# Kernel tuning notes

Hardware: AMD Instinct MI355X
Metric: run time of the kernel (lower is better)

The kernel has to match this reference:

```python
import jax, jax.numpy as jnp
import numpy as np

NUM_TEAMS = 100000
INPUT_SIZE = 128
HIDDEN = 128
NUM_MATCHES = 1000000
OUT = 3


def setup_inputs() -> dict:
    key = jax.random.key(0)
    ks = jax.random.split(key, 10)
    s_ih = 1.0 / np.sqrt(HIDDEN)
    inputs = jax.random.normal(ks[0], (NUM_TEAMS, INPUT_SIZE), dtype=jnp.float32)
    hx = jax.random.normal(ks[1], (NUM_TEAMS, HIDDEN), dtype=jnp.float32)
    cx = jax.random.normal(ks[2], (NUM_TEAMS, HIDDEN), dtype=jnp.float32)
    matches = jax.random.randint(ks[3], (NUM_MATCHES, 2), 0, NUM_TEAMS, dtype=jnp.int64)
    W_ih = jax.random.uniform(ks[4], (4 * HIDDEN, INPUT_SIZE), jnp.float32, -s_ih, s_ih)
    W_hh = jax.random.uniform(ks[5], (4 * HIDDEN, HIDDEN), jnp.float32, -s_ih, s_ih)
    b_ih = jax.random.uniform(ks[6], (4 * HIDDEN,), jnp.float32, -s_ih, s_ih)
    b_hh = jax.random.uniform(ks[7], (4 * HIDDEN,), jnp.float32, -s_ih, s_ih)
    s_o = 1.0 / np.sqrt(2 * HIDDEN)
    W_out = jax.random.uniform(ks[8], (OUT, 2 * HIDDEN), jnp.float32, -s_o, s_o)
    b_out = jax.random.uniform(ks[9], (OUT,), jnp.float32, -s_o, s_o)
    return {"inputs": inputs, "hx": hx, "cx": cx, "matches": matches,
            "W_ih": W_ih, "W_hh": W_hh, "b_ih": b_ih, "b_hh": b_hh,
            "W_out": W_out, "b_out": b_out}


def reference(inputs, hx, cx, matches, W_ih, W_hh, b_ih, b_hh, W_out, b_out):
    # Batched LSTMCell step across all teams (replaces per-team Python loop).
    gates = inputs @ W_ih.T + b_ih + hx @ W_hh.T + b_hh  # [T, 4H]
    i_g, f_g, g_g, o_g = jnp.split(gates, 4, axis=1)
    c_new = jax.nn.sigmoid(f_g) * cx + jax.nn.sigmoid(i_g) * jnp.tanh(g_g)
    h_new = jax.nn.sigmoid(o_g) * jnp.tanh(c_new)  # [T, H]
    # Fused gather + concat + linear + softmax for all matches.
    home = h_new[matches[:, 0]]  # [M, H]
    away = h_new[matches[:, 1]]  # [M, H]
    feat = jnp.concatenate([home, away], axis=1)  # [M, 2H]
    logits = feat @ W_out.T + b_out  # [M, 3]
    pmf = jax.nn.softmax(logits, axis=-1)
    return pmf
```

## Files before the change

kernel.cpp:

```cpp
#include <hip/hip_runtime.h>
#include <hip/hip_bf16.h>

typedef __bf16 bf16x8 __attribute__((ext_vector_type(8)));
typedef float f32x4 __attribute__((ext_vector_type(4)));

#define NUM_TEAMS 100000
#define NUM_MATCHES 1000000
#define LOG2E 1.4426950408889634f
#define NWG 1563
#define XQ 195
#define XR 3

__device__ __forceinline__ unsigned short f2bf(float x) {
    __hip_bfloat16 h = __float2bfloat16(x);
    return reinterpret_cast<unsigned short&>(h);
}
__device__ __forceinline__ unsigned int cvtpk(float a, float b) {
    unsigned int r;
    asm("v_cvt_pk_bf16_f32 %0, %1, %2" : "=v"(r) : "v"(a), "v"(b));
    return r;
}
__device__ __forceinline__ float exp2_(float x) {
    float r; asm("v_exp_f32 %0, %1" : "=v"(r) : "v"(x)); return r;
}
__device__ __forceinline__ float rcp_(float x) {
    float r; asm("v_rcp_f32 %0, %1" : "=v"(r) : "v"(x)); return r;
}
__device__ __forceinline__ void load_lds16(const float* g, float* l) {
    __builtin_amdgcn_global_load_lds(
        (const __attribute__((address_space(1))) void*)g,
        (__attribute__((address_space(3))) void*)l, 16, 0, 0);
}

__global__ __launch_bounds__(256) void prep_kernel(
    const float* __restrict__ W_ih, const float* __restrict__ W_hh,
    const float* __restrict__ b_ih, const float* __restrict__ b_hh,
    unsigned short* __restrict__ Wpk, float* __restrict__ biasc)
{
    int gid = blockIdx.x * 256 + threadIdx.x;
    int e = gid & 7;
    int chunk = gid >> 3;
    int l15 = chunk & 15;
    int l4 = (chunk >> 4) & 3;
    int rest = chunk >> 6;
    int ks = rest & 7;
    int gate = (rest >> 3) & 3;
    int G = rest >> 5;
    int row = gate * 128 + G * 16 + l15;
    int k = ks * 32 + l4 * 8 + e;
    float v = (k < 128) ? W_ih[row * 128 + k] : W_hh[row * 128 + (k - 128)];
    Wpk[gid] = f2bf(v);
    if (gid < 512) {
        float b = b_ih[gid] + b_hh[gid];
        float scale = ((gid >> 7) == 2) ? (2.0f * LOG2E) : (-LOG2E);
        biasc[gid] = b * scale;
    }
}

__global__ __launch_bounds__(512, 4) void lstm_kernel(
    const float* __restrict__ inputs, const float* __restrict__ hx,
    const float* __restrict__ cx, const unsigned short* __restrict__ Wpk,
    const float* __restrict__ biasc, const float* __restrict__ W_out,
    float* __restrict__ projP)
{
    __shared__ __align__(16) float Af[64 * 256];
    __shared__ float Wlds[768];
    const int tid = threadIdx.x;

    const int orig = blockIdx.x;
    const int xcd = orig & 7, idx = orig >> 3;
    const int tile = (xcd < XR ? xcd * (XQ + 1) : XR * (XQ + 1) + (xcd - XR) * XQ) + idx;
    const int brow = tile * 64;

    const int lane = tid & 63;
    const int w = tid >> 6;
    const int l15 = lane & 15, l4 = lane >> 4;
    const int hcol = w * 16 + l15;

    {
        const int su = lane ^ w;
        const int col = su * 4;
        const float* base = (col < 128) ? inputs + col : hx + (col - 128);
        #pragma unroll
        for (int p = 0; p < 8; ++p) {
            int row = p * 8 + w;
            int team = brow + row; if (team >= NUM_TEAMS) team = NUM_TEAMS - 1;
            load_lds16(base + (size_t)team * 128, Af + row * 256 + lane * 4);
        }
        Wlds[tid] = W_out[tid];
        if (tid < 256) Wlds[512 + tid] = W_out[512 + tid];
    }

    const unsigned short* bpg = Wpk + (size_t)w * 16384 + lane * 8;
    const float bic = biasc[hcol];
    const float bfc = biasc[128 + hcol];
    const float bgc = biasc[256 + hcol];
    const float boc = biasc[384 + hcol];
    const int u0 = ((l4 * 2) ^ (l15 & 7)) << 4;
    const int u1 = ((l4 * 2 + 1) ^ (l15 & 7)) << 4;

    f32x4 acc[4][4] = {};

    asm volatile("s_waitcnt vmcnt(0)" ::: "memory");
    __syncthreads();

    const char* Ab = reinterpret_cast<const char*>(Af);
    #pragma unroll
    for (int ks = 0; ks < 8; ++ks) {
        bf16x8 b0 = *(const bf16x8*)(bpg + ks * 512);
        bf16x8 b1 = *(const bf16x8*)(bpg + 4096 + ks * 512);
        bf16x8 b2 = *(const bf16x8*)(bpg + 8192 + ks * 512);
        bf16x8 b3 = *(const bf16x8*)(bpg + 12288 + ks * 512);
        #pragma unroll
        for (int m = 0; m < 4; ++m) {
            const char* pa = Ab + (m * 16 + l15) * 1024 + ks * 128;
            f32x4 a0 = *reinterpret_cast<const f32x4*>(pa + u0);
            f32x4 a1 = *reinterpret_cast<const f32x4*>(pa + u1);
            union { uint4 q; bf16x8 v; } cc;
            cc.q.x = cvtpk(a0[0], a0[1]);
            cc.q.y = cvtpk(a0[2], a0[3]);
            cc.q.z = cvtpk(a1[0], a1[1]);
            cc.q.w = cvtpk(a1[2], a1[3]);
            bf16x8 af = cc.v;
            acc[m][0] = __builtin_amdgcn_mfma_f32_16x16x32_bf16(af, b0, acc[m][0], 0, 0, 0);
            acc[m][1] = __builtin_amdgcn_mfma_f32_16x16x32_bf16(af, b1, acc[m][1], 0, 0, 0);
            acc[m][2] = __builtin_amdgcn_mfma_f32_16x16x32_bf16(af, b2, acc[m][2], 0, 0, 0);
            acc[m][3] = __builtin_amdgcn_mfma_f32_16x16x32_bf16(af, b3, acc[m][3], 0, 0, 0);
        }
    }

    float cxa[16];
    #pragma unroll
    for (int m = 0; m < 4; ++m)
        #pragma unroll
        for (int j = 0; j < 4; ++j) {
            int team = brow + m * 16 + l4 * 4 + j;
            if (team >= NUM_TEAMS) team = NUM_TEAMS - 1;
            cxa[m * 4 + j] = cx[(size_t)team * 128 + hcol];
        }

    __syncthreads();

    {
        char* lb = reinterpret_cast<char*>(Af);
        #pragma unroll
        for (int m = 0; m < 4; ++m) {
            #pragma unroll
            for (int j = 0; j < 4; ++j) {
                float si = rcp_(1.0f + exp2_(fmaf(acc[m][0][j], -LOG2E, bic)));
                float sf = rcp_(1.0f + exp2_(fmaf(acc[m][1][j], -LOG2E, bfc)));
                float tg = fmaf(-2.0f, rcp_(1.0f + exp2_(fmaf(acc[m][2][j], 2.0f * LOG2E, bgc))), 1.0f);
                float so = rcp_(1.0f + exp2_(fmaf(acc[m][3][j], -LOG2E, boc)));
                float cn = fmaf(sf, cxa[m * 4 + j], si * tg);
                float tc = fmaf(-2.0f, rcp_(1.0f + exp2_(cn * (2.0f * LOG2E))), 1.0f);
                float hn = so * tc;
                int t = m * 16 + l4 * 4 + j;
                *reinterpret_cast<float*>(lb + ((t * 512 + hcol * 4) ^ ((t & 7) << 4))) = hn;
            }
        }
    }
    __syncthreads();

    {
        int tl = tid >> 3, sub = tid & 7;
        const char* lb = reinterpret_cast<const char*>(Af);
        int hbase = tl * 512 + sub * 64;
        int hswz = (tl & 7) << 4;
        float a0 = 0.f, a1 = 0.f, a2 = 0.f, a3 = 0.f, a4 = 0.f, a5 = 0.f;
        #pragma unroll
        for (int c = 0; c < 4; ++c) {
            f32x4 h4 = *reinterpret_cast<const f32x4*>(lb + ((hbase + c * 16) ^ hswz));
            #pragma unroll
            for (int i = 0; i < 4; ++i) {
                float h = h4[i];
                int col = sub * 16 + c * 4 + i;
                a0 += h * Wlds[col];       a1 += h * Wlds[256 + col]; a2 += h * Wlds[512 + col];
                a3 += h * Wlds[128 + col]; a4 += h * Wlds[384 + col]; a5 += h * Wlds[640 + col];
            }
        }
        a0 += __shfl_xor(a0, 1); a1 += __shfl_xor(a1, 1); a2 += __shfl_xor(a2, 1);
        a3 += __shfl_xor(a3, 1); a4 += __shfl_xor(a4, 1); a5 += __shfl_xor(a5, 1);
        a0 += __shfl_xor(a0, 2); a1 += __shfl_xor(a1, 2); a2 += __shfl_xor(a2, 2);
        a3 += __shfl_xor(a3, 2); a4 += __shfl_xor(a4, 2); a5 += __shfl_xor(a5, 2);
        a0 += __shfl_xor(a0, 4); a1 += __shfl_xor(a1, 4); a2 += __shfl_xor(a2, 4);
        a3 += __shfl_xor(a3, 4); a4 += __shfl_xor(a4, 4); a5 += __shfl_xor(a5, 4);
        int team = brow + tl;
        if (sub == 0 && team < NUM_TEAMS) {
            float4* o = reinterpret_cast<float4*>(projP + (size_t)team * 8);
            o[0] = make_float4(a0, a1, a2, a2);
            o[1] = make_float4(a3, a4, a5, a5);
        }
    }
}

__global__ __launch_bounds__(256) void match_kernel(
    const int* __restrict__ matches, const float* __restrict__ projP,
    const float* __restrict__ b_out, float* __restrict__ out)
{
    int m = blockIdx.x * 256 + threadIdx.x;
    if (m >= NUM_MATCHES) return;
    int2 mi = reinterpret_cast<const int2*>(matches)[m];
    const float4* pp = reinterpret_cast<const float4*>(projP);
    float4 hv = pp[(size_t)mi.x * 2 + 0];
    float4 av = pp[(size_t)mi.y * 2 + 1];
    float l0 = hv.x + av.x + b_out[0];
    float l1 = hv.y + av.y + b_out[1];
    float l2 = hv.z + av.z + b_out[2];
    float mx = fmaxf(l0, fmaxf(l1, l2));
    float e0 = __expf(l0 - mx), e1 = __expf(l1 - mx), e2 = __expf(l2 - mx);
    float inv = 1.0f / (e0 + e1 + e2);
    out[3 * m + 0] = e0 * inv;
    out[3 * m + 1] = e1 * inv;
    out[3 * m + 2] = e2 * inv;
}

extern "C" void kernel_launch(void* const* d_in, const int* in_sizes, int n_in,
                              void* d_out, int out_size, void* d_ws, size_t ws_size,
                              hipStream_t stream) {
    const float* inputs = (const float*)d_in[0];
    const float* hx     = (const float*)d_in[1];
    const float* cx     = (const float*)d_in[2];
    const int*   matches= (const int*)d_in[3];
    const float* W_ih   = (const float*)d_in[4];
    const float* W_hh   = (const float*)d_in[5];
    const float* b_ih   = (const float*)d_in[6];
    const float* b_hh   = (const float*)d_in[7];
    const float* W_out  = (const float*)d_in[8];
    const float* b_out  = (const float*)d_in[9];
    float* out = (float*)d_out;

    char* ws = (char*)d_ws;
    unsigned short* Wpk  = (unsigned short*)ws;
    float* biasc         = (float*)(ws + 262144);
    float* projP         = (float*)(ws + (1 << 20));

    prep_kernel <<<512, 256, 0, stream>>>(W_ih, W_hh, b_ih, b_hh, Wpk, biasc);
    lstm_kernel <<<NWG, 512, 0, stream>>>(inputs, hx, cx, Wpk, biasc, W_out, projP);
    match_kernel<<<(NUM_MATCHES + 255) / 256, 256, 0, stream>>>(matches, projP, b_out, out);
}
```

Baseline: 80.34 us.

## Make LSTM kernel persistent with double-buffered LDS tile prefetch and register-resident weights

The LSTM kernel now launches a fixed grid of 256 workgroups that loop over the 64-row team tiles. While one tile is computed, the next tile's inputs/hx are loaded into a second LDS buffer. The bf16 gate-weight fragments are loaded into registers once per workgroup instead of once per tile, and some barriers become lgkmcnt-only waits. The intent is to remove per-workgroup launch and weight-reload overhead and hide load latency. The trade-offs are that the doubled LDS use and launch bound of 2 cut occupancy, and 1563 tiles over 256 workgroups leaves the last wave of tiles unbalanced.

```diff
diff --git a/kernel.cpp b/kernel.cpp
--- a/kernel.cpp
+++ b/kernel.cpp
@@ -7,9 +7,8 @@
 #define NUM_TEAMS 100000
 #define NUM_MATCHES 1000000
 #define LOG2E 1.4426950408889634f
-#define NWG 1563
-#define XQ 195
-#define XR 3
+#define NTILES 1563
+#define GRID 256
 
 __device__ __forceinline__ unsigned short f2bf(float x) {
     __hip_bfloat16 h = __float2bfloat16(x);
@@ -30,6 +29,12 @@
     __builtin_amdgcn_global_load_lds(
         (const __attribute__((address_space(1))) void*)g,
         (__attribute__((address_space(3))) void*)l, 16, 0, 0);
+}
+__device__ __forceinline__ void barrier_lgkm() {
+    asm volatile("s_waitcnt lgkmcnt(0)" ::: "memory");
+    __builtin_amdgcn_sched_barrier(0);
+    __builtin_amdgcn_s_barrier();
+    __builtin_amdgcn_sched_barrier(0);
 }
 
 __global__ __launch_bounds__(256) void prep_kernel(
@@ -57,139 +62,153 @@
     }
 }
 
-__global__ __launch_bounds__(512, 4) void lstm_kernel(
+__global__ __launch_bounds__(512, 2) void lstm_kernel(
     const float* __restrict__ inputs, const float* __restrict__ hx,
     const float* __restrict__ cx, const unsigned short* __restrict__ Wpk,
     const float* __restrict__ biasc, const float* __restrict__ W_out,
     float* __restrict__ projP)
 {
-    __shared__ __align__(16) float Af[64 * 256];
+    __shared__ __align__(16) float Af[2][64 * 256];
     __shared__ float Wlds[768];
     const int tid = threadIdx.x;
-
-    const int orig = blockIdx.x;
-    const int xcd = orig & 7, idx = orig >> 3;
-    const int tile = (xcd < XR ? xcd * (XQ + 1) : XR * (XQ + 1) + (xcd - XR) * XQ) + idx;
-    const int brow = tile * 64;
-
     const int lane = tid & 63;
     const int w = tid >> 6;
     const int l15 = lane & 15, l4 = lane >> 4;
     const int hcol = w * 16 + l15;
 
-    {
-        const int su = lane ^ w;
-        const int col = su * 4;
-        const float* base = (col < 128) ? inputs + col : hx + (col - 128);
-        #pragma unroll
-        for (int p = 0; p < 8; ++p) {
-            int row = p * 8 + w;
-            int team = brow + row; if (team >= NUM_TEAMS) team = NUM_TEAMS - 1;
-            load_lds16(base + (size_t)team * 128, Af + row * 256 + lane * 4);
-        }
-        Wlds[tid] = W_out[tid];
-        if (tid < 256) Wlds[512 + tid] = W_out[512 + tid];
-    }
-
     const unsigned short* bpg = Wpk + (size_t)w * 16384 + lane * 8;
+    bf16x8 Bf[4][8];
+    #pragma unroll
+    for (int g = 0; g < 4; ++g)
+        #pragma unroll
+        for (int ks = 0; ks < 8; ++ks)
+            Bf[g][ks] = *(const bf16x8*)(bpg + g * 4096 + ks * 512);
+
     const float bic = biasc[hcol];
     const float bfc = biasc[128 + hcol];
     const float bgc = biasc[256 + hcol];
     const float boc = biasc[384 + hcol];
+
+    Wlds[tid] = W_out[tid];
+    if (tid < 256) Wlds[512 + tid] = W_out[512 + tid];
+
+    const int su = lane ^ w;
+    const int scol = su * 4;
+    const float* sbase = (scol < 128) ? inputs + scol : hx + (scol - 128);
     const int u0 = ((l4 * 2) ^ (l15 & 7)) << 4;
     const int u1 = ((l4 * 2 + 1) ^ (l15 & 7)) << 4;
 
-    f32x4 acc[4][4] = {};
-
-    asm volatile("s_waitcnt vmcnt(0)" ::: "memory");
-    __syncthreads();
-
-    const char* Ab = reinterpret_cast<const char*>(Af);
-    #pragma unroll
-    for (int ks = 0; ks < 8; ++ks) {
-        bf16x8 b0 = *(const bf16x8*)(bpg + ks * 512);
-        bf16x8 b1 = *(const bf16x8*)(bpg + 4096 + ks * 512);
-        bf16x8 b2 = *(const bf16x8*)(bpg + 8192 + ks * 512);
-        bf16x8 b3 = *(const bf16x8*)(bpg + 12288 + ks * 512);
-        #pragma unroll
-        for (int m = 0; m < 4; ++m) {
-            const char* pa = Ab + (m * 16 + l15) * 1024 + ks * 128;
-            f32x4 a0 = *reinterpret_cast<const f32x4*>(pa + u0);
-            f32x4 a1 = *reinterpret_cast<const f32x4*>(pa + u1);
-            union { uint4 q; bf16x8 v; } cc;
-            cc.q.x = cvtpk(a0[0], a0[1]);
-            cc.q.y = cvtpk(a0[2], a0[3]);
-            cc.q.z = cvtpk(a1[0], a1[1]);
-            cc.q.w = cvtpk(a1[2], a1[3]);
-            bf16x8 af = cc.v;
-            acc[m][0] = __builtin_amdgcn_mfma_f32_16x16x32_bf16(af, b0, acc[m][0], 0, 0, 0);
-            acc[m][1] = __builtin_amdgcn_mfma_f32_16x16x32_bf16(af, b1, acc[m][1], 0, 0, 0);
-            acc[m][2] = __builtin_amdgcn_mfma_f32_16x16x32_bf16(af, b2, acc[m][2], 0, 0, 0);
-            acc[m][3] = __builtin_amdgcn_mfma_f32_16x16x32_bf16(af, b3, acc[m][3], 0, 0, 0);
-        }
-    }
-
-    float cxa[16];
-    #pragma unroll
-    for (int m = 0; m < 4; ++m)
-        #pragma unroll
-        for (int j = 0; j < 4; ++j) {
-            int team = brow + m * 16 + l4 * 4 + j;
-            if (team >= NUM_TEAMS) team = NUM_TEAMS - 1;
-            cxa[m * 4 + j] = cx[(size_t)team * 128 + hcol];
-        }
-
-    __syncthreads();
-
+    const int t0 = blockIdx.x;
     {
-        char* lb = reinterpret_cast<char*>(Af);
-        #pragma unroll
-        for (int m = 0; m < 4; ++m) {
-            #pragma unroll
-            for (int j = 0; j < 4; ++j) {
-                float si = rcp_(1.0f + exp2_(fmaf(acc[m][0][j], -LOG2E, bic)));
-                float sf = rcp_(1.0f + exp2_(fmaf(acc[m][1][j], -LOG2E, bfc)));
-                float tg = fmaf(-2.0f, rcp_(1.0f + exp2_(fmaf(acc[m][2][j], 2.0f * LOG2E, bgc))), 1.0f);
-                float so = rcp_(1.0f + exp2_(fmaf(acc[m][3][j], -LOG2E, boc)));
-                float cn = fmaf(sf, cxa[m * 4 + j], si * tg);
-                float tc = fmaf(-2.0f, rcp_(1.0f + exp2_(cn * (2.0f * LOG2E))), 1.0f);
-                float hn = so * tc;
-                int t = m * 16 + l4 * 4 + j;
-                *reinterpret_cast<float*>(lb + ((t * 512 + hcol * 4) ^ ((t & 7) << 4))) = hn;
-            }
+        float* buf = &Af[0][0];
+        #pragma unroll
+        for (int p = 0; p < 8; ++p) {
+            int row = p * 8 + w;
+            int team = t0 * 64 + row; if (team >= NUM_TEAMS) team = NUM_TEAMS - 1;
+            load_lds16(sbase + (size_t)team * 128, buf + row * 256 + lane * 4);
         }
     }
     __syncthreads();
 
-    {
-        int tl = tid >> 3, sub = tid & 7;
-        const char* lb = reinterpret_cast<const char*>(Af);
-        int hbase = tl * 512 + sub * 64;
-        int hswz = (tl & 7) << 4;
-        float a0 = 0.f, a1 = 0.f, a2 = 0.f, a3 = 0.f, a4 = 0.f, a5 = 0.f;
-        #pragma unroll
-        for (int c = 0; c < 4; ++c) {
-            f32x4 h4 = *reinterpret_cast<const f32x4*>(lb + ((hbase + c * 16) ^ hswz));
-            #pragma unroll
-            for (int i = 0; i < 4; ++i) {
-                float h = h4[i];
-                int col = sub * 16 + c * 4 + i;
-                a0 += h * Wlds[col];       a1 += h * Wlds[256 + col]; a2 += h * Wlds[512 + col];
-                a3 += h * Wlds[128 + col]; a4 += h * Wlds[384 + col]; a5 += h * Wlds[640 + col];
-            }
-        }
-        a0 += __shfl_xor(a0, 1); a1 += __shfl_xor(a1, 1); a2 += __shfl_xor(a2, 1);
-        a3 += __shfl_xor(a3, 1); a4 += __shfl_xor(a4, 1); a5 += __shfl_xor(a5, 1);
-        a0 += __shfl_xor(a0, 2); a1 += __shfl_xor(a1, 2); a2 += __shfl_xor(a2, 2);
-        a3 += __shfl_xor(a3, 2); a4 += __shfl_xor(a4, 2); a5 += __shfl_xor(a5, 2);
-        a0 += __shfl_xor(a0, 4); a1 += __shfl_xor(a1, 4); a2 += __shfl_xor(a2, 4);
-        a3 += __shfl_xor(a3, 4); a4 += __shfl_xor(a4, 4); a5 += __shfl_xor(a5, 4);
-        int team = brow + tl;
-        if (sub == 0 && team < NUM_TEAMS) {
-            float4* o = reinterpret_cast<float4*>(projP + (size_t)team * 8);
-            o[0] = make_float4(a0, a1, a2, a2);
-            o[1] = make_float4(a3, a4, a5, a5);
-        }
+    int cur = 0;
+    for (int t = t0; t < NTILES; t += GRID, cur ^= 1) {
+        const int brow = t * 64;
+
+        if (t + GRID < NTILES) {
+            float* buf = &Af[cur ^ 1][0];
+            const int tb = (t + GRID) * 64;
+            #pragma unroll
+            for (int p = 0; p < 8; ++p) {
+                int row = p * 8 + w;
+                int team = tb + row; if (team >= NUM_TEAMS) team = NUM_TEAMS - 1;
+                load_lds16(sbase + (size_t)team * 128, buf + row * 256 + lane * 4);
+            }
+        }
+        float cxa[16];
+        #pragma unroll
+        for (int m = 0; m < 4; ++m)
+            #pragma unroll
+            for (int j = 0; j < 4; ++j) {
+                int team = brow + m * 16 + l4 * 4 + j;
+                if (team >= NUM_TEAMS) team = NUM_TEAMS - 1;
+                cxa[m * 4 + j] = cx[(size_t)team * 128 + hcol];
+            }
+
+        f32x4 acc[4][4] = {};
+        const char* Ab = reinterpret_cast<const char*>(&Af[cur][0]);
+        #pragma unroll
+        for (int ks = 0; ks < 8; ++ks) {
+            #pragma unroll
+            for (int m = 0; m < 4; ++m) {
+                const char* pa = Ab + (m * 16 + l15) * 1024 + ks * 128;
+                f32x4 a0 = *reinterpret_cast<const f32x4*>(pa + u0);
+                f32x4 a1 = *reinterpret_cast<const f32x4*>(pa + u1);
+                union { uint4 q; bf16x8 v; } cc;
+                cc.q.x = cvtpk(a0[0], a0[1]);
+                cc.q.y = cvtpk(a0[2], a0[3]);
+                cc.q.z = cvtpk(a1[0], a1[1]);
+                cc.q.w = cvtpk(a1[2], a1[3]);
+                bf16x8 af = cc.v;
+                acc[m][0] = __builtin_amdgcn_mfma_f32_16x16x32_bf16(af, Bf[0][ks], acc[m][0], 0, 0, 0);
+                acc[m][1] = __builtin_amdgcn_mfma_f32_16x16x32_bf16(af, Bf[1][ks], acc[m][1], 0, 0, 0);
+                acc[m][2] = __builtin_amdgcn_mfma_f32_16x16x32_bf16(af, Bf[2][ks], acc[m][2], 0, 0, 0);
+                acc[m][3] = __builtin_amdgcn_mfma_f32_16x16x32_bf16(af, Bf[3][ks], acc[m][3], 0, 0, 0);
+            }
+        }
+
+        barrier_lgkm();
+
+        {
+            char* lb = reinterpret_cast<char*>(&Af[cur][0]);
+            #pragma unroll
+            for (int m = 0; m < 4; ++m) {
+                #pragma unroll
+                for (int j = 0; j < 4; ++j) {
+                    float si = rcp_(1.0f + exp2_(fmaf(acc[m][0][j], -LOG2E, bic)));
+                    float sf = rcp_(1.0f + exp2_(fmaf(acc[m][1][j], -LOG2E, bfc)));
+                    float tg = fmaf(-2.0f, rcp_(1.0f + exp2_(fmaf(acc[m][2][j], 2.0f * LOG2E, bgc))), 1.0f);
+                    float so = rcp_(1.0f + exp2_(fmaf(acc[m][3][j], -LOG2E, boc)));
+                    float cn = fmaf(sf, cxa[m * 4 + j], si * tg);
+                    float tc = fmaf(-2.0f, rcp_(1.0f + exp2_(cn * (2.0f * LOG2E))), 1.0f);
+                    float hn = so * tc;
+                    int tl = m * 16 + l4 * 4 + j;
+                    *reinterpret_cast<float*>(lb + ((tl * 512 + hcol * 4) ^ ((tl & 7) << 4))) = hn;
+                }
+            }
+        }
+        barrier_lgkm();
+
+        {
+            int tl = tid >> 3, sub = tid & 7;
+            const char* lb = reinterpret_cast<const char*>(&Af[cur][0]);
+            int hbase = tl * 512 + sub * 64;
+            int hswz = (tl & 7) << 4;
+            float a0 = 0.f, a1 = 0.f, a2 = 0.f, a3 = 0.f, a4 = 0.f, a5 = 0.f;
+            #pragma unroll
+            for (int c = 0; c < 4; ++c) {
+                f32x4 h4 = *reinterpret_cast<const f32x4*>(lb + ((hbase + c * 16) ^ hswz));
+                #pragma unroll
+                for (int i = 0; i < 4; ++i) {
+                    float h = h4[i];
+                    int col = sub * 16 + c * 4 + i;
+                    a0 += h * Wlds[col];       a1 += h * Wlds[256 + col]; a2 += h * Wlds[512 + col];
+                    a3 += h * Wlds[128 + col]; a4 += h * Wlds[384 + col]; a5 += h * Wlds[640 + col];
+                }
+            }
+            a0 += __shfl_xor(a0, 1); a1 += __shfl_xor(a1, 1); a2 += __shfl_xor(a2, 1);
+            a3 += __shfl_xor(a3, 1); a4 += __shfl_xor(a4, 1); a5 += __shfl_xor(a5, 1);
+            a0 += __shfl_xor(a0, 2); a1 += __shfl_xor(a1, 2); a2 += __shfl_xor(a2, 2);
+            a3 += __shfl_xor(a3, 2); a4 += __shfl_xor(a4, 2); a5 += __shfl_xor(a5, 2);
+            a0 += __shfl_xor(a0, 4); a1 += __shfl_xor(a1, 4); a2 += __shfl_xor(a2, 4);
+            a3 += __shfl_xor(a3, 4); a4 += __shfl_xor(a4, 4); a5 += __shfl_xor(a5, 4);
+            int team = brow + tl;
+            if (sub == 0 && team < NUM_TEAMS) {
+                float4* o = reinterpret_cast<float4*>(projP + (size_t)team * 8);
+                o[0] = make_float4(a0, a1, a2, a2);
+                o[1] = make_float4(a3, a4, a5, a5);
+            }
+        }
+        __syncthreads();
     }
 }
 
@@ -235,6 +254,6 @@
     float* projP         = (float*)(ws + (1 << 20));
 
     prep_kernel <<<512, 256, 0, stream>>>(W_ih, W_hh, b_ih, b_hh, Wpk, biasc);
-    lstm_kernel <<<NWG, 512, 0, stream>>>(inputs, hx, cx, Wpk, biasc, W_out, projP);
+    lstm_kernel <<<GRID, 512, 0, stream>>>(inputs, hx, cx, Wpk, biasc, W_out, projP);
     match_kernel<<<(NUM_MATCHES + 255) / 256, 256, 0, stream>>>(matches, projP, b_out, out);
 }
```

After: 150.5 us. 1.87x slower.
